# Optimization experiments

Measured on AMD Instinct MI355X. Metric: run time of the kernel, lower is better.

Reference implementation:

```python
import jax, jax.numpy as jnp
import numpy as np

B, C, F_, NUM_STEPS = 8, 256, 16384, 20
EPS = 1e-5


def setup_inputs() -> dict:
    key = jax.random.key(0)
    k1, k2, k3, k4 = jax.random.split(key, 4)
    x = jax.random.normal(k1, (B, C, F_), jnp.float32)
    f = jnp.arange(F_)
    # triangle-mesh-like adjacency with log-diameter so BFS terminates in <= ~log2(F)+2 levels
    adj1 = jnp.stack([(f + 1) % F_, (2 * f) % F_, (2 * f + 1) % F_], axis=1)
    adj = jnp.broadcast_to(adj1, (B, F_, 3)).astype(jnp.int32)
    anchors = jax.random.randint(k2, (B,), 0, F_).astype(jnp.int32)
    W_conv = jax.random.normal(k3, (4 * C, C), jnp.float32) / np.sqrt(4 * C).astype(np.float32)
    b_conv = jnp.zeros((C,), jnp.float32)
    W_mlp = jax.random.normal(k4, (C, 1), jnp.float32) / np.sqrt(C).astype(np.float32)
    b_mlp = jnp.zeros((1,), jnp.float32)
    return dict(x=x, adj=adj, anchors=anchors, W_conv=W_conv, b_conv=b_conv, W_mlp=W_mlp, b_mlp=b_mlp)


def reference(x, adj, anchors, W_conv, b_conv, W_mlp, b_mlp):
    feats = jnp.swapaxes(x, 1, 2)  # [B, F, C]
    # init_scores = mlp(x.transpose(2,1)): Linear(C,1) + Sigmoid
    init_scores = jax.nn.sigmoid(feats @ W_mlp + b_mlp)[..., 0]  # [B, F]

    def per_mesh(feat, adj_m, anchor, isc):
        nF = feat.shape[0]
        # gather [self | 3 neighbors] features -> [F, 4C] (reads original features, so precompute once)
        g = jnp.concatenate([feat[:, None, :], feat[adj_m]], axis=1).reshape(nF, 4 * C)
        h = g @ W_conv + b_conv                              # Linear(4C -> C)
        h = (h - h.mean(-1, keepdims=True)) / jnp.sqrt(h.var(-1, keepdims=True) + EPS)  # InstanceNorm1d (no affine)
        pred = jax.nn.sigmoid(h @ W_mlp + b_mlp)[:, 0]       # [F] scores in (0,1)

        done0 = jnp.zeros((nF,), bool).at[anchor].set(True)
        adj_flat = adj_m.reshape(-1)

        def step(carry, _):
            scores, done, boundary = carry
            nb_done = done[adj_m]                            # [F,3] visited neighbors
            nb_sc = jnp.where(nb_done, scores[adj_m], -1.0)  # scores live in [0,1]
            nbmax = jnp.where(nb_done.any(1), nb_sc.max(1), 1.0)
            new = jnp.minimum(jnp.maximum(pred, scores), nbmax)
            scores = jnp.where(boundary, new, scores)
            done2 = done | boundary
            reach = jnp.zeros((nF,), jnp.int32).at[adj_flat].max(jnp.repeat(boundary, 3).astype(jnp.int32))
            boundary2 = (reach > 0) & ~done2                 # next BFS frontier
            return (scores, done2, boundary2), None

        (scores, done, _), _ = jax.lax.scan(step, (isc, done0, done0), None, length=NUM_STEPS)
        out_feat = jnp.where(done[:, None], h, feat)         # visited faces get conv features
        return out_feat, scores[:, None]

    final_features, final_scores = jax.vmap(per_mesh)(feats, adj, anchors, init_scores)
    return final_features, final_scores
```

## Files before the change

kernel.cpp:

```cpp
#include <hip/hip_runtime.h>
#include <math.h>

#define NB 8
#define NC 256
#define NF 16384
#define NSTEPS 20

typedef unsigned short u16;
typedef unsigned int u32;
typedef __bf16 bf16x8 __attribute__((ext_vector_type(8)));
typedef float f32x4 __attribute__((ext_vector_type(4)));

__device__ __forceinline__ u16 f2bf(float f) {
    u32 u = __float_as_uint(f);
    u += 0x7fffu + ((u >> 16) & 1u);
    return (u16)(u >> 16);
}

__global__ void prep_w_kernel(const float* __restrict__ Wc, u16* __restrict__ Wt) {
    int i = blockIdx.x * 256 + threadIdx.x;
    int n = i >> 10, k = i & 1023;
    Wt[i] = f2bf(Wc[k * 256 + n]);
}

__global__ __launch_bounds__(256) void transpose_kernel(
    const float* __restrict__ x, u16* __restrict__ featsT,
    const float* __restrict__ W_mlp, float* __restrict__ partS) {
    __shared__ float tile[64][69];
    __shared__ float psum[64][4];
    int ft = blockIdx.x, ct = blockIdx.y, b = blockIdx.z;
    int t = threadIdx.x;
    int r = t >> 2, cg = t & 3;

    const float* xp = x + ((size_t)(b * 256 + ct * 64 + r)) * NF + ft * 64 + cg * 16;
    float4 v0 = *(const float4*)(xp + 0);
    float4 v1 = *(const float4*)(xp + 4);
    float4 v2 = *(const float4*)(xp + 8);
    float4 v3 = *(const float4*)(xp + 12);
    float* tr = &tile[r][cg * 16];
    tr[0] = v0.x; tr[1] = v0.y; tr[2]  = v0.z; tr[3]  = v0.w;
    tr[4] = v1.x; tr[5] = v1.y; tr[6]  = v1.z; tr[7]  = v1.w;
    tr[8] = v2.x; tr[9] = v2.y; tr[10] = v2.z; tr[11] = v2.w;
    tr[12] = v3.x; tr[13] = v3.y; tr[14] = v3.z; tr[15] = v3.w;
    __syncthreads();

    int fl = t >> 2;
    int c0 = cg * 16;
    float part = 0.f;
    u16 tmp[16];
#pragma unroll
    for (int j = 0; j < 16; ++j) {
        float v = tile[c0 + j][fl];
        part += v * W_mlp[ct * 64 + c0 + j];
        tmp[j] = f2bf(v);
    }
    u16* dst = featsT + ((size_t)(b * NF + ft * 64 + fl)) * 256 + ct * 64 + c0;
    u32 u[8];
#pragma unroll
    for (int j = 0; j < 8; ++j) u[j] = (u32)tmp[2 * j] | ((u32)tmp[2 * j + 1] << 16);
    uint4 p0; p0.x = u[0]; p0.y = u[1]; p0.z = u[2]; p0.w = u[3];
    uint4 p1; p1.x = u[4]; p1.y = u[5]; p1.z = u[6]; p1.w = u[7];
    *(uint4*)dst = p0;
    *(uint4*)(dst + 8) = p1;

    psum[fl][cg] = part;
    __syncthreads();
    if (t < 64) {
        float s = psum[t][0] + psum[t][1] + psum[t][2] + psum[t][3];
        partS[((size_t)(b * NF + ft * 64 + t)) * 4 + ct] = s;
    }
}

__global__ void init_scores_kernel(const float* __restrict__ partS,
                                   const float* __restrict__ b_mlp,
                                   float* __restrict__ sc) {
    int i = blockIdx.x * 256 + threadIdx.x;
    float s = partS[i * 4] + partS[i * 4 + 1] + partS[i * 4 + 2] + partS[i * 4 + 3] + b_mlp[0];
    sc[i] = 1.f / (1.f + expf(-s));
}

__global__ __launch_bounds__(512) void conv_gemm_kernel(
    const u16* __restrict__ featsT, const u16* __restrict__ Wt,
    const float* __restrict__ b_conv, const float* __restrict__ W_mlp,
    const float* __restrict__ b_mlp, const int* __restrict__ adj,
    float* __restrict__ out_feat, float* __restrict__ pred) {
    __shared__ __align__(16) u16 Albs[128 * 64];
    __shared__ __align__(16) u16 Blbs[256 * 64];
    __shared__ int srcIdx[128 * 4];
    __shared__ float red[128 * 4 * 2];
    __shared__ float mstd[128 * 2];

    int bx = blockIdx.x;
    int b = bx >> 7;
    int f0 = (bx & 127) << 7;
    int tid = threadIdx.x;
    int w = tid >> 6, lane = tid & 63;
    int wm = w >> 2, wn = w & 3;
    const int c16 = lane & 15, q4 = lane >> 4;

    if (tid < 128) {
        int f = f0 + tid;
        const int* ap = adj + ((size_t)(b * NF + f)) * 3;
        srcIdx[tid * 4 + 0] = f;
        srcIdx[tid * 4 + 1] = ap[0];
        srcIdx[tid * 4 + 2] = ap[1];
        srcIdx[tid * 4 + 3] = ap[2];
    }
    f32x4 acc[4][4] = {};
    const size_t meshBase = (size_t)b * NF * 256;
    __syncthreads();

    for (int kk = 0; kk < 16; ++kk) {
        int slot = kk >> 2;
        int ch0 = (kk & 3) << 6;
#pragma unroll
        for (int p = 0; p < 2; ++p) {
            int rrow = ((w * 2 + p) << 3) + (lane >> 3);
            int c8 = lane & 7;
            int src = srcIdx[rrow * 4 + slot];
            const u16* gp = featsT + meshBase + (size_t)src * 256 + ch0 + ((c8 ^ (rrow & 7)) << 3);
            __builtin_amdgcn_global_load_lds((const __attribute__((address_space(1))) void*)gp,
                                             (__attribute__((address_space(3))) void*)&Albs[(w * 2 + p) * 512],
                                             16, 0, 0);
        }
#pragma unroll
        for (int p = 0; p < 4; ++p) {
            int n = ((w * 4 + p) << 3) + (lane >> 3);
            int c8 = lane & 7;
            const u16* gp = Wt + n * 1024 + (kk << 6) + ((c8 ^ (n & 7)) << 3);
            __builtin_amdgcn_global_load_lds((const __attribute__((address_space(1))) void*)gp,
                                             (__attribute__((address_space(3))) void*)&Blbs[(w * 4 + p) * 512],
                                             16, 0, 0);
        }
        __syncthreads();
#pragma unroll
        for (int kh = 0; kh < 2; ++kh) {
            int k8 = (kh << 2) + q4;
            bf16x8 af[4], bfr[4];
#pragma unroll
            for (int mi = 0; mi < 4; ++mi) {
                int m = (wm << 6) + (mi << 4) + c16;
                af[mi] = *(const bf16x8*)&Albs[(m << 6) + ((k8 ^ (m & 7)) << 3)];
            }
#pragma unroll
            for (int ni = 0; ni < 4; ++ni) {
                int n = (wn << 6) + (ni << 4) + c16;
                bfr[ni] = *(const bf16x8*)&Blbs[(n << 6) + ((k8 ^ (n & 7)) << 3)];
            }
#pragma unroll
            for (int mi = 0; mi < 4; ++mi)
#pragma unroll
                for (int ni = 0; ni < 4; ++ni)
                    acc[mi][ni] = __builtin_amdgcn_mfma_f32_16x16x32_bf16(af[mi], bfr[ni], acc[mi][ni], 0, 0, 0);
        }
        __syncthreads();
    }

    float bcv[4], wml[4];
#pragma unroll
    for (int ni = 0; ni < 4; ++ni) {
        int col = (wn << 6) + (ni << 4) + c16;
        bcv[ni] = b_conv[col];
        wml[ni] = W_mlp[col];
    }
    float s[4][4], q2[4][4];
#pragma unroll
    for (int mi = 0; mi < 4; ++mi)
#pragma unroll
        for (int r = 0; r < 4; ++r) {
            float ss = 0.f, qq = 0.f;
#pragma unroll
            for (int ni = 0; ni < 4; ++ni) {
                float v = acc[mi][ni][r] + bcv[ni];
                acc[mi][ni][r] = v;
                ss += v; qq += v * v;
            }
            s[mi][r] = ss; q2[mi][r] = qq;
        }
#pragma unroll
    for (int msk = 1; msk < 16; msk <<= 1)
#pragma unroll
        for (int mi = 0; mi < 4; ++mi)
#pragma unroll
            for (int r = 0; r < 4; ++r) {
                s[mi][r] += __shfl_xor(s[mi][r], msk);
                q2[mi][r] += __shfl_xor(q2[mi][r], msk);
            }
    if (c16 == 0) {
#pragma unroll
        for (int mi = 0; mi < 4; ++mi)
#pragma unroll
            for (int r = 0; r < 4; ++r) {
                int row = (wm << 6) + (mi << 4) + (q4 << 2) + r;
                red[(row * 4 + wn) * 2 + 0] = s[mi][r];
                red[(row * 4 + wn) * 2 + 1] = q2[mi][r];
            }
    }
    __syncthreads();
    if (tid < 128) {
        float ss = red[tid * 8 + 0] + red[tid * 8 + 2] + red[tid * 8 + 4] + red[tid * 8 + 6];
        float qq = red[tid * 8 + 1] + red[tid * 8 + 3] + red[tid * 8 + 5] + red[tid * 8 + 7];
        float mean = ss * (1.f / 256.f);
        float var = qq * (1.f / 256.f) - mean * mean;
        mstd[tid * 2 + 0] = mean;
        mstd[tid * 2 + 1] = rsqrtf(var + 1e-5f);
    }
    __syncthreads();
    float ps[4][4];
#pragma unroll
    for (int mi = 0; mi < 4; ++mi)
#pragma unroll
        for (int r = 0; r < 4; ++r) {
            int row = (wm << 6) + (mi << 4) + (q4 << 2) + r;
            float mean = mstd[row * 2], rstd = mstd[row * 2 + 1];
            float* op = out_feat + meshBase + (size_t)(f0 + row) * 256 + (wn << 6) + c16;
            float pp = 0.f;
#pragma unroll
            for (int ni = 0; ni < 4; ++ni) {
                float hn = (acc[mi][ni][r] - mean) * rstd;
                op[ni << 4] = hn;
                pp += hn * wml[ni];
            }
            ps[mi][r] = pp;
        }
#pragma unroll
    for (int msk = 1; msk < 16; msk <<= 1)
#pragma unroll
        for (int mi = 0; mi < 4; ++mi)
#pragma unroll
            for (int r = 0; r < 4; ++r)
                ps[mi][r] += __shfl_xor(ps[mi][r], msk);
    if (c16 == 0) {
#pragma unroll
        for (int mi = 0; mi < 4; ++mi)
#pragma unroll
            for (int r = 0; r < 4; ++r) {
                int row = (wm << 6) + (mi << 4) + (q4 << 2) + r;
                red[row * 4 + wn] = ps[mi][r];
            }
    }
    __syncthreads();
    if (tid < 128) {
        float t = red[tid * 4] + red[tid * 4 + 1] + red[tid * 4 + 2] + red[tid * 4 + 3] + b_mlp[0];
        pred[b * NF + f0 + tid] = 1.f / (1.f + expf(-t));
    }
}

__global__ __launch_bounds__(1024) void bfs_kernel(
    const int* __restrict__ adj, const int* __restrict__ anchors,
    const float* __restrict__ pred, float* __restrict__ sc,
    u32* __restrict__ doneOut) {
    __shared__ u32 done[512], bnd[512], nxt[512];
    int b = blockIdx.x, tid = threadIdx.x;
    if (tid < 512) { done[tid] = 0u; bnd[tid] = 0u; }
    __syncthreads();
    if (tid == 0) {
        int a = anchors[b];
        done[a >> 5] |= 1u << (a & 31);
        bnd[a >> 5] |= 1u << (a & 31);
    }
    const int* adjb = adj + (size_t)b * NF * 3;
    const float* pb = pred + b * NF;
    float* scb = sc + b * NF;
    __syncthreads();
    for (int step = 0; step < NSTEPS; ++step) {
        if (tid < 512) nxt[tid] = 0u;
        __syncthreads();
        for (int i = 0; i < 16; ++i) {
            int f = tid + (i << 10);
            if ((bnd[f >> 5] >> (f & 31)) & 1u) {
                int a0 = adjb[f * 3 + 0], a1 = adjb[f * 3 + 1], a2 = adjb[f * 3 + 2];
                bool d0 = (done[a0 >> 5] >> (a0 & 31)) & 1u;
                bool d1 = (done[a1 >> 5] >> (a1 & 31)) & 1u;
                bool d2 = (done[a2 >> 5] >> (a2 & 31)) & 1u;
                float nb = -1.f;
                if (d0) nb = fmaxf(nb, scb[a0]);
                if (d1) nb = fmaxf(nb, scb[a1]);
                if (d2) nb = fmaxf(nb, scb[a2]);
                if (!(d0 | d1 | d2)) nb = 1.f;
                float nv = fminf(fmaxf(pb[f], scb[f]), nb);
                scb[f] = nv;
                atomicOr(&nxt[a0 >> 5], 1u << (a0 & 31));
                atomicOr(&nxt[a1 >> 5], 1u << (a1 & 31));
                atomicOr(&nxt[a2 >> 5], 1u << (a2 & 31));
            }
        }
        __syncthreads();
        if (tid < 512) {
            u32 d2w = done[tid] | bnd[tid];
            done[tid] = d2w;
            bnd[tid] = nxt[tid] & ~d2w;
        }
        __syncthreads();
    }
    if (tid < 512) doneOut[b * 512 + tid] = done[tid];
}

__global__ void fixup_kernel(const float* __restrict__ x, const u32* __restrict__ doneBits,
                             float* __restrict__ out_feat) {
    int b = blockIdx.y;
    int f = (blockIdx.x << 8) + threadIdx.x;
    if (!((doneBits[b * 512 + (f >> 5)] >> (f & 31)) & 1u)) {
        float* op = out_feat + ((size_t)(b * NF + f)) * 256;
        const float* xp = x + (size_t)b * 256 * NF + f;
        for (int cc = 0; cc < 256; ++cc) op[cc] = xp[(size_t)cc * NF];
    }
}

extern "C" void kernel_launch(void* const* d_in, const int* in_sizes, int n_in,
                              void* d_out, int out_size, void* d_ws, size_t ws_size,
                              hipStream_t stream) {
    const float* x = (const float*)d_in[0];
    const int* adj = (const int*)d_in[1];
    const int* anchors = (const int*)d_in[2];
    const float* W_conv = (const float*)d_in[3];
    const float* b_conv = (const float*)d_in[4];
    const float* W_mlp = (const float*)d_in[5];
    const float* b_mlp = (const float*)d_in[6];

    float* out_feat = (float*)d_out;
    float* out_sc = out_feat + (size_t)NB * NF * 256;

    char* wsp = (char*)d_ws;
    u16* featsT = (u16*)wsp;  wsp += (size_t)NB * NF * 256 * 2;
    u16* Wt = (u16*)wsp;      wsp += (size_t)256 * 1024 * 2;
    float* partS = (float*)wsp; wsp += (size_t)NB * NF * 4 * 4;
    float* pred = (float*)wsp;  wsp += (size_t)NB * NF * 4;
    u32* doneBits = (u32*)wsp;  wsp += (size_t)NB * 512 * 4;

    prep_w_kernel<<<1024, 256, 0, stream>>>(W_conv, Wt);
    transpose_kernel<<<dim3(256, 4, NB), 256, 0, stream>>>(x, featsT, W_mlp, partS);
    init_scores_kernel<<<512, 256, 0, stream>>>(partS, b_mlp, out_sc);
    conv_gemm_kernel<<<1024, 512, 0, stream>>>(featsT, Wt, b_conv, W_mlp, b_mlp, adj, out_feat, pred);
    bfs_kernel<<<NB, 1024, 0, stream>>>(adj, anchors, pred, out_sc, doneBits);
    fixup_kernel<<<dim3(64, NB), 256, 0, stream>>>(x, doneBits, out_feat);
}
```

Baseline: 435.1 us.

## Alias GEMM LDS buffers for occupancy and switch BFS to compact frontier queues

The conv GEMM kernel now overlays its reduction and mean/std scratch on the A/B tile LDS buffers, adds a barrier so the reuse is safe, and asks for 4 waves-per-EU occupancy via launch bounds. The goal is lower LDS and register footprint so more blocks fit per CU. Separately, the BFS kernel replaces the full 16K-face bitmap scan each step with explicit frontier queues in global memory, filled through LDS atomics on a seen bitmap. Work per step then scales with frontier size, at the cost of atomic counter contention and extra queue traffic.

```diff
diff --git a/kernel.cpp b/kernel.cpp
--- a/kernel.cpp
+++ b/kernel.cpp
@@ -79,16 +79,17 @@
     sc[i] = 1.f / (1.f + expf(-s));
 }
 
-__global__ __launch_bounds__(512) void conv_gemm_kernel(
+__global__ __launch_bounds__(512, 4) void conv_gemm_kernel(
     const u16* __restrict__ featsT, const u16* __restrict__ Wt,
     const float* __restrict__ b_conv, const float* __restrict__ W_mlp,
     const float* __restrict__ b_mlp, const int* __restrict__ adj,
     float* __restrict__ out_feat, float* __restrict__ pred) {
-    __shared__ __align__(16) u16 Albs[128 * 64];
-    __shared__ __align__(16) u16 Blbs[256 * 64];
+    __shared__ __align__(16) u16 AB[128 * 64 + 256 * 64];
     __shared__ int srcIdx[128 * 4];
-    __shared__ float red[128 * 4 * 2];
-    __shared__ float mstd[128 * 2];
+    u16* Albs = AB;
+    u16* Blbs = AB + 128 * 64;
+    float* red = (float*)AB;
+    float* mstd = (float*)AB + 1024;
 
     int bx = blockIdx.x;
     int b = bx >> 7;
@@ -230,6 +231,7 @@
 #pragma unroll
             for (int r = 0; r < 4; ++r)
                 ps[mi][r] += __shfl_xor(ps[mi][r], msk);
+    __syncthreads();
     if (c16 == 0) {
 #pragma unroll
         for (int mi = 0; mi < 4; ++mi)
@@ -249,49 +251,56 @@
 __global__ __launch_bounds__(1024) void bfs_kernel(
     const int* __restrict__ adj, const int* __restrict__ anchors,
     const float* __restrict__ pred, float* __restrict__ sc,
-    u32* __restrict__ doneOut) {
-    __shared__ u32 done[512], bnd[512], nxt[512];
+    u32* __restrict__ doneOut, int* __restrict__ qbuf) {
+    __shared__ u32 done[512], seen[512];
+    __shared__ int cntCur, cntNext;
     int b = blockIdx.x, tid = threadIdx.x;
-    if (tid < 512) { done[tid] = 0u; bnd[tid] = 0u; }
+    if (tid < 512) { done[tid] = 0u; seen[tid] = 0u; }
+    if (tid == 0) { cntCur = 1; cntNext = 0; }
+    int* q0 = qbuf + (size_t)b * 2 * NF;
+    int* q1 = q0 + NF;
+    const int* adjb = adj + (size_t)b * NF * 3;
+    const float* pb = pred + b * NF;
+    float* scb = sc + b * NF;
     __syncthreads();
     if (tid == 0) {
         int a = anchors[b];
         done[a >> 5] |= 1u << (a & 31);
-        bnd[a >> 5] |= 1u << (a & 31);
-    }
-    const int* adjb = adj + (size_t)b * NF * 3;
-    const float* pb = pred + b * NF;
-    float* scb = sc + b * NF;
-    __syncthreads();
+        seen[a >> 5] |= 1u << (a & 31);
+        q0[0] = a;
+    }
+    __syncthreads();
+    int* qc = q0;
+    int* qn = q1;
     for (int step = 0; step < NSTEPS; ++step) {
-        if (tid < 512) nxt[tid] = 0u;
+        int n = cntCur;
+        for (int i = tid; i < n; i += 1024) {
+            int f = qc[i];
+            int a0 = adjb[f * 3 + 0], a1 = adjb[f * 3 + 1], a2 = adjb[f * 3 + 2];
+            bool d0 = (done[a0 >> 5] >> (a0 & 31)) & 1u;
+            bool d1 = (done[a1 >> 5] >> (a1 & 31)) & 1u;
+            bool d2 = (done[a2 >> 5] >> (a2 & 31)) & 1u;
+            float nb = -1.f;
+            if (d0) nb = fmaxf(nb, scb[a0]);
+            if (d1) nb = fmaxf(nb, scb[a1]);
+            if (d2) nb = fmaxf(nb, scb[a2]);
+            if (!(d0 | d1 | d2)) nb = 1.f;
+            scb[f] = fminf(fmaxf(pb[f], scb[f]), nb);
+            u32 m0 = 1u << (a0 & 31);
+            if (!(atomicOr(&seen[a0 >> 5], m0) & m0)) qn[atomicAdd(&cntNext, 1)] = a0;
+            u32 m1 = 1u << (a1 & 31);
+            if (!(atomicOr(&seen[a1 >> 5], m1) & m1)) qn[atomicAdd(&cntNext, 1)] = a1;
+            u32 m2 = 1u << (a2 & 31);
+            if (!(atomicOr(&seen[a2 >> 5], m2) & m2)) qn[atomicAdd(&cntNext, 1)] = a2;
+        }
         __syncthreads();
-        for (int i = 0; i < 16; ++i) {
-            int f = tid + (i << 10);
-            if ((bnd[f >> 5] >> (f & 31)) & 1u) {
-                int a0 = adjb[f * 3 + 0], a1 = adjb[f * 3 + 1], a2 = adjb[f * 3 + 2];
-                bool d0 = (done[a0 >> 5] >> (a0 & 31)) & 1u;
-                bool d1 = (done[a1 >> 5] >> (a1 & 31)) & 1u;
-                bool d2 = (done[a2 >> 5] >> (a2 & 31)) & 1u;
-                float nb = -1.f;
-                if (d0) nb = fmaxf(nb, scb[a0]);
-                if (d1) nb = fmaxf(nb, scb[a1]);
-                if (d2) nb = fmaxf(nb, scb[a2]);
-                if (!(d0 | d1 | d2)) nb = 1.f;
-                float nv = fminf(fmaxf(pb[f], scb[f]), nb);
-                scb[f] = nv;
-                atomicOr(&nxt[a0 >> 5], 1u << (a0 & 31));
-                atomicOr(&nxt[a1 >> 5], 1u << (a1 & 31));
-                atomicOr(&nxt[a2 >> 5], 1u << (a2 & 31));
-            }
-        }
+        for (int i = tid; i < n; i += 1024) {
+            int f = qc[i];
+            atomicOr(&done[f >> 5], 1u << (f & 31));
+        }
+        if (tid == 0) { cntCur = cntNext; cntNext = 0; }
         __syncthreads();
-        if (tid < 512) {
-            u32 d2w = done[tid] | bnd[tid];
-            done[tid] = d2w;
-            bnd[tid] = nxt[tid] & ~d2w;
-        }
-        __syncthreads();
+        int* t = qc; qc = qn; qn = t;
     }
     if (tid < 512) doneOut[b * 512 + tid] = done[tid];
 }
@@ -327,11 +336,12 @@
     float* partS = (float*)wsp; wsp += (size_t)NB * NF * 4 * 4;
     float* pred = (float*)wsp;  wsp += (size_t)NB * NF * 4;
     u32* doneBits = (u32*)wsp;  wsp += (size_t)NB * 512 * 4;
+    int* qbuf = (int*)wsp;      wsp += (size_t)NB * 2 * NF * 4;
 
     prep_w_kernel<<<1024, 256, 0, stream>>>(W_conv, Wt);
     transpose_kernel<<<dim3(256, 4, NB), 256, 0, stream>>>(x, featsT, W_mlp, partS);
     init_scores_kernel<<<512, 256, 0, stream>>>(partS, b_mlp, out_sc);
     conv_gemm_kernel<<<1024, 512, 0, stream>>>(featsT, Wt, b_conv, W_mlp, b_mlp, adj, out_feat, pred);
-    bfs_kernel<<<NB, 1024, 0, stream>>>(adj, anchors, pred, out_sc, doneBits);
+    bfs_kernel<<<NB, 1024, 0, stream>>>(adj, anchors, pred, out_sc, doneBits, qbuf);
     fixup_kernel<<<dim3(64, NB), 256, 0, stream>>>(x, doneBits, out_feat);
 }
```

Measured after the change: 444.2 us. 2.1% more time.
